# Kernel tuning notes

Hardware: AMD Instinct MI355X
Metric: run time of the kernel (lower is better)

## Reference

```python
import jax, jax.numpy as jnp
import numpy as np

VOCAB = 100000
E = 256      # embedding dim == projection dim (required by layer-axis concat)
H = 2048     # lstm hidden dim
P = 256      # projection dim
B, T = 8, 96
CELL_CLIP = 3.0
PROJ_CLIP = 3.0
NUM_LAYERS = 2


def setup_inputs() -> dict:
    key = jax.random.key(0)
    ks = jax.random.split(key, 8)
    tokens = jax.random.randint(ks[0], (B, T), 0, VOCAB, dtype=jnp.int32)
    mask = jnp.ones((B, T, 1), dtype=jnp.float32)
    embed_table = jax.random.normal(ks[1], (VOCAB + 1, E), dtype=jnp.float32) * 0.05
    # stacked LSTM weights: index 0=fwd L0, 1=fwd L1, 2=bwd L0, 3=bwd L1
    Wk = jax.random.normal(ks[2], (4, E, 4 * H), dtype=jnp.float32) * 0.02
    Wr = jax.random.normal(ks[3], (4, P, 4 * H), dtype=jnp.float32) * 0.02
    b = jnp.zeros((4, 4 * H), dtype=jnp.float32)
    Wp = jax.random.normal(ks[4], (4, H, P), dtype=jnp.float32) * 0.02
    elmo_w = jnp.zeros((NUM_LAYERS + 1,), dtype=jnp.float32)
    gamma = jnp.ones((1,), dtype=jnp.float32)
    return {"tokens": tokens, "mask": mask, "embed_table": embed_table,
            "Wk": Wk, "Wr": Wr, "b": b, "Wp": Wp,
            "elmo_w": elmo_w, "gamma": gamma}


def _lstm_proj(x, m, Wk, Wr, b, Wp, reverse):
    # x: [B,T,E], m: [B,T,1]. LSTM with cell clip, output projection, proj clip.
    if reverse:
        x = jnp.flip(x, 1)
        m = jnp.flip(m, 1)
    xs = jnp.swapaxes(x, 0, 1)                     # [T,B,E]
    ms = jnp.swapaxes(m, 0, 1)                     # [T,B,1]
    xW = jnp.einsum('tbe,ef->tbf', xs, Wk) + b     # precompute input gates [T,B,4H]

    def step(carry, inp):
        h, c = carry                               # h:[B,P], c:[B,H]
        zx, mt = inp
        z = zx + h @ Wr                            # [B,4H]
        i, f, g, o = jnp.split(z, 4, axis=-1)
        i = jax.nn.sigmoid(i)
        f = jax.nn.sigmoid(f)
        g = jnp.tanh(g)
        o = jax.nn.sigmoid(o)
        c_new = jnp.clip(f * c + i * g, -CELL_CLIP, CELL_CLIP)
        h_new = jnp.clip((o * jnp.tanh(c_new)) @ Wp, -PROJ_CLIP, PROJ_CLIP)
        keep = mt > 0
        h_new = jnp.where(keep, h_new, h)
        c_new = jnp.where(keep, c_new, c)
        return (h_new, c_new), h_new

    h0 = jnp.zeros((x.shape[0], Wp.shape[1]), x.dtype)
    c0 = jnp.zeros((x.shape[0], Wp.shape[0]), x.dtype)
    _, hs = jax.lax.scan(step, (h0, c0), (xW, ms))
    out = jnp.swapaxes(hs, 0, 1)                   # [B,T,P]
    if reverse:
        out = jnp.flip(out, 1)
    return out


def _elmo_layers(tokens, mask, embed_table, Wk, Wr, b, Wp):
    emb = embed_table[tokens]                      # [B,T,E]
    dir_outs = []
    for rev, base in ((False, 0), (True, 2)):
        inp = emb
        outs = []
        for l in range(NUM_LAYERS):
            out = _lstm_proj(inp, mask, Wk[base + l], Wr[base + l],
                             b[base + l], Wp[base + l], rev)
            inp = inp + out if l > 0 else out      # skip connection on layer > 0
            outs.append(inp)
        dir_outs.append(outs)
    fwd, bwd = dir_outs
    layers = [jnp.concatenate([emb, emb], -1)]
    layers += [jnp.concatenate([f, bb], -1) for f, bb in zip(fwd, bwd)]
    return jnp.stack(layers, axis=1)               # [B, L+1, T, 2P]


def reference(tokens, mask, embed_table, Wk, Wr, b, Wp, elmo_w, gamma):
    all_emb = _elmo_layers(tokens, mask, embed_table, Wk, Wr, b, Wp)
    m = mask[:, None, :, :]                        # [B,1,T,1]
    num = jnp.sum(mask, axis=(1, 2))[:, None]      # [B,1]
    xm = all_emb * m
    mean = jnp.sum(xm, axis=(2, 3)) / num          # [B,L+1]
    mean = mean[:, :, None, None]
    var = jnp.sum(((xm - mean) * m) ** 2, axis=(2, 3)) / num
    var = var[:, :, None, None]
    normed = (all_emb - mean) / jnp.sqrt(var + 1e-12)
    w = jax.nn.softmax(elmo_w)[None, :, None, None]
    weighted = jnp.sum(w * normed, axis=1) * gamma  # [B,T,2P]
    return weighted
```

## Files before the change

### kernel.cpp

```cpp
#include <hip/hip_runtime.h>
#include <hip/hip_bf16.h>

#define DEVFN __device__ __forceinline__

static constexpr size_t OFF_CTRS   = 0;
static constexpr size_t OFF_FLAG   = 131072;
static constexpr size_t OFF_STATS  = 131328;
static constexpr size_t OFF_EW     = 131584;
static constexpr size_t OFF_MASK32 = 131840;
static constexpr size_t OFF_EMB    = 135168;
static constexpr size_t OFF_WPT    = 921600;
static constexpr size_t OFF_BIAS   = 9310208;
static constexpr size_t OFF_XW     = 9441280;
static constexpr size_t OFF_OUT0   = 59772928;
static constexpr size_t OFF_OUT1   = 61345792;
static constexpr size_t OFF_Y      = 62918656;
static constexpr size_t OFF_H      = 75501568;

template<int BF>
DEVFN float ldin(const void* p, size_t i) {
  if (BF) {
    unsigned short u = ((const unsigned short*)p)[i];
    return __uint_as_float(((unsigned)u) << 16);
  }
  return ((const float*)p)[i];
}
DEVFN float ldraw(const void* p, size_t i, int bf) {
  if (bf) {
    unsigned short u = ((const unsigned short*)p)[i];
    return __uint_as_float(((unsigned)u) << 16);
  }
  return ((const float*)p)[i];
}

DEVFN float sigm(float x) { return 1.f / (1.f + __expf(-x)); }
DEVFN float clip3(float x) { return fminf(fmaxf(x, -3.f), 3.f); }

__global__ void detect_k(const unsigned* mask_raw, int* flagp) {
  if (threadIdx.x == 0) *flagp = (mask_raw[0] == 0x3F800000u) ? 0 : 1;
}

template<int BF>
__global__ void convert_k(const int* flagp, const void* bias, const void* mask,
                          const void* ew, const void* gm,
                          float* bias32, float* mask32, float* ew32) {
  if (*flagp != BF) return;
  size_t i = (size_t)blockIdx.x * 256 + threadIdx.x;
  if (i >= 33540) return;
  if (i < 32768)       bias32[i] = ldin<BF>(bias, i);
  else if (i < 33536)  mask32[i - 32768] = ldin<BF>(mask, i - 32768);
  else if (i < 33539)  ew32[i - 33536]   = ldin<BF>(ew, i - 33536);
  else                 ew32[3] = ldin<BF>(gm, 0);
}

template<int BF>
__global__ void transpose_wp_k(const int* flagp, const void* Wp, float* WpT) {
  if (*flagp != BF) return;
  const int kt = blockIdx.x, pt = blockIdx.y, dl = blockIdx.z;
  __shared__ float tile[64][65];
  const int tid = threadIdx.x;
  for (int it = 0; it < 4; ++it) {
    int lin = it * 1024 + tid * 4;
    int kk = lin >> 6, pp = lin & 63;
    size_t src = ((size_t)(dl * 2048 + kt * 64 + kk)) * 256 + pt * 64 + pp;
    float v0, v1, v2, v3;
    if (BF) {
      const unsigned short* sp = (const unsigned short*)Wp + src;
      v0 = __uint_as_float(((unsigned)sp[0]) << 16);
      v1 = __uint_as_float(((unsigned)sp[1]) << 16);
      v2 = __uint_as_float(((unsigned)sp[2]) << 16);
      v3 = __uint_as_float(((unsigned)sp[3]) << 16);
    } else {
      float4 v = *(const float4*)((const float*)Wp + src);
      v0 = v.x; v1 = v.y; v2 = v.z; v3 = v.w;
    }
    tile[pp + 0][kk] = v0; tile[pp + 1][kk] = v1; tile[pp + 2][kk] = v2; tile[pp + 3][kk] = v3;
  }
  __syncthreads();
  for (int it = 0; it < 4; ++it) {
    int lin = it * 1024 + tid * 4;
    int pr = lin >> 6, kc = lin & 63;
    float4 o;
    o.x = tile[pr][kc + 0]; o.y = tile[pr][kc + 1]; o.z = tile[pr][kc + 2]; o.w = tile[pr][kc + 3];
    *(float4*)(WpT + ((size_t)(dl * 256 + pt * 64 + pr)) * 2048 + kt * 64 + kc) = o;
  }
}

template<int BF>
__global__ void gather_k(const int* flagp, const int* tokens, const void* et, float* emb) {
  if (*flagp != BF) return;
  const int bt = blockIdx.x;
  const int tok = tokens[bt];
  emb[(size_t)bt * 256 + threadIdx.x] = ldin<BF>(et, (size_t)tok * 256 + threadIdx.x);
}

template<int BF>
__global__ __launch_bounds__(256) void xw_gemm_k(
    const int* __restrict__ flagp, const float* __restrict__ x_fwd, const float* __restrict__ x_bwd,
    const void* __restrict__ Wk, const float* __restrict__ bias32, float* __restrict__ xW, int layer) {
  if (*flagp != BF) return;
  const int nt = blockIdx.x, mt = blockIdx.y, dir = blockIdx.z;
  const int dl = dir * 2 + layer;
  const float* xb = dir ? x_bwd : x_fwd;
  const int tid = threadIdx.x;

  __shared__ float As[16][68];
  __shared__ float Bs[16][68];

  float acc[4][4] = {};
  const int tx = tid & 15, ty = tid >> 4;

  const int am = tid >> 2;
  const int ak = (tid & 3) * 4;
  const int m_glob = mt * 64 + am;
  const int t_ = m_glob >> 3, b_ = m_glob & 7;
  const int tau = dir ? (95 - t_) : t_;
  const float* arow = xb + ((size_t)(b_ * 96 + tau)) * 256;

  const int bk = tid >> 4, bn = (tid & 15) * 4;

  for (int kb = 0; kb < 256; kb += 16) {
    float4 av = *(const float4*)(arow + kb + ak);
    As[ak + 0][am] = av.x; As[ak + 1][am] = av.y; As[ak + 2][am] = av.z; As[ak + 3][am] = av.w;

    size_t bidx = ((size_t)dl * 256 + (kb + bk)) * 8192 + (size_t)nt * 64 + bn;
    float b0, b1, b2, b3;
    if (BF) {
      ushort4 uv = *(const ushort4*)((const unsigned short*)Wk + bidx);
      b0 = __uint_as_float(((unsigned)uv.x) << 16);
      b1 = __uint_as_float(((unsigned)uv.y) << 16);
      b2 = __uint_as_float(((unsigned)uv.z) << 16);
      b3 = __uint_as_float(((unsigned)uv.w) << 16);
    } else {
      float4 fv = *(const float4*)((const float*)Wk + bidx);
      b0 = fv.x; b1 = fv.y; b2 = fv.z; b3 = fv.w;
    }
    Bs[bk][bn + 0] = b0; Bs[bk][bn + 1] = b1; Bs[bk][bn + 2] = b2; Bs[bk][bn + 3] = b3;
    __syncthreads();

#pragma unroll
    for (int kk = 0; kk < 16; ++kk) {
      float a0 = As[kk][ty * 4 + 0], a1 = As[kk][ty * 4 + 1], a2 = As[kk][ty * 4 + 2], a3 = As[kk][ty * 4 + 3];
      float c0 = Bs[kk][tx * 4 + 0], c1 = Bs[kk][tx * 4 + 1], c2 = Bs[kk][tx * 4 + 2], c3 = Bs[kk][tx * 4 + 3];
      acc[0][0] = fmaf(a0, c0, acc[0][0]); acc[0][1] = fmaf(a0, c1, acc[0][1]);
      acc[0][2] = fmaf(a0, c2, acc[0][2]); acc[0][3] = fmaf(a0, c3, acc[0][3]);
      acc[1][0] = fmaf(a1, c0, acc[1][0]); acc[1][1] = fmaf(a1, c1, acc[1][1]);
      acc[1][2] = fmaf(a1, c2, acc[1][2]); acc[1][3] = fmaf(a1, c3, acc[1][3]);
      acc[2][0] = fmaf(a2, c0, acc[2][0]); acc[2][1] = fmaf(a2, c1, acc[2][1]);
      acc[2][2] = fmaf(a2, c2, acc[2][2]); acc[2][3] = fmaf(a2, c3, acc[2][3]);
      acc[3][0] = fmaf(a3, c0, acc[3][0]); acc[3][1] = fmaf(a3, c1, acc[3][1]);
      acc[3][2] = fmaf(a3, c2, acc[3][2]); acc[3][3] = fmaf(a3, c3, acc[3][3]);
    }
    __syncthreads();
  }

  const int n0 = nt * 64 + tx * 4;
#pragma unroll
  for (int i = 0; i < 4; ++i) {
    int m = mt * 64 + ty * 4 + i;
    int tt = m >> 3, bb = m & 7;
    float4 o;
    o.x = acc[i][0] + bias32[dl * 8192 + n0 + 0];
    o.y = acc[i][1] + bias32[dl * 8192 + n0 + 1];
    o.z = acc[i][2] + bias32[dl * 8192 + n0 + 2];
    o.w = acc[i][3] + bias32[dl * 8192 + n0 + 3];
    *(float4*)(xW + (size_t)((dir * 96 + tt) * 8 + bb) * 8192 + n0) = o;
  }
}


__global__ __launch_bounds__(256, 2) void scan_kernel(
    const float* __restrict__ xW, const void* __restrict__ WrRaw, const int* __restrict__ flagp,
    const float* __restrict__ WpT, const float* __restrict__ mask32,
    float* __restrict__ out, float* __restrict__ hbuf, float* __restrict__ ybuf,
    int* ctrs, int layer) {
  const int tid = threadIdx.x;
  const int w = blockIdx.x;
  const int dir = w >> 8;
  const int g = w & 255;
  const int dl = dir * 2 + layer;

  __shared__ __align__(16) float wr_s[256 * 32];
  __shared__ __align__(16) float h_lds[2048];
  __shared__ float4 wp4_s[512];
  __shared__ float4 zpart[288];
  __shared__ float  z_s[32 * 9];
  __shared__ __align__(16) float xw_s[256];
  __shared__ float  mask_s[768];
  __shared__ float  c_s[64];
  __shared__ float  red_s[8];

  int* base = ctrs + (layer * 2 + dir) * 65 * 64;
  int* aline = base + (g >> 2) * 64;
  int ep = 0;
  const int bf = *flagp;

  {
    const size_t wrbase = (size_t)dl * 256 * 8192;
    for (int i = tid; i < 8192; i += 256) {
      int k = i >> 5, col = i & 31;
      wr_s[i] = ldraw(WrRaw, wrbase + (size_t)k * 8192 + (size_t)(col >> 3) * 2048 + g * 8 + (col & 7), bf);
    }
    const float4* wrow = (const float4*)(WpT + ((size_t)(dl * 256 + g)) * 2048);
    for (int i = tid; i < 512; i += 256) wp4_s[i] = wrow[i];
    for (int i = tid; i < 768; i += 256) mask_s[i] = mask32[i];
  }
  if (tid < 64) c_s[tid] = 0.f;

  const int ks = tid >> 6, colq = (tid >> 3) & 7, lb = tid & 7;
  const float4* wr4 = (const float4*)wr_s;
  const float4* xw4 = (const float4*)xw_s;
  int* myline = base + (tid & 63) * 64;

  for (int t = 0; t < 96; ++t) {
    const int tau = dir ? (95 - t) : t;
    const float* h_cur = hbuf + ((size_t)(t * 2 + dir)) * 2048;
    float* h_nxt = hbuf + ((size_t)((t + 1) * 2 + dir)) * 2048;
    float* y_t   = ybuf + ((size_t)(t * 2 + dir)) * 16384;

    float xwv;
    {
      int b = tid >> 5, col = tid & 31;
      xwv = xW[(size_t)((dir * 96 + t) * 8 + b) * 8192 + (col >> 3) * 2048 + g * 8 + (col & 7)];
    }

    if (t == 0) {
      ((float4*)h_lds)[tid * 2 + 0] = make_float4(0.f, 0.f, 0.f, 0.f);
      ((float4*)h_lds)[tid * 2 + 1] = make_float4(0.f, 0.f, 0.f, 0.f);
    } else {
      ((float4*)h_lds)[tid * 2 + 0] = ((const float4*)h_cur)[tid * 2 + 0];
      ((float4*)h_lds)[tid * 2 + 1] = ((const float4*)h_cur)[tid * 2 + 1];
    }
    __syncthreads();

    {
      float4 acc = make_float4(0.f, 0.f, 0.f, 0.f);
#pragma unroll 16
      for (int i = 0; i < 64; ++i) {
        int k = (ks << 6) + i;
        float hv = h_lds[k * 8 + lb];
        float4 wv = wr4[k * 8 + colq];
        acc.x = fmaf(hv, wv.x, acc.x); acc.y = fmaf(hv, wv.y, acc.y);
        acc.z = fmaf(hv, wv.z, acc.z); acc.w = fmaf(hv, wv.w, acc.w);
      }
      zpart[(ks * 8 + colq) * 9 + lb] = acc;
      xw_s[tid] = xwv;
    }
    __syncthreads();

    ++ep;
    if (tid < 64) {
      {
        const int b3 = tid & 7, cq = tid >> 3;
        float4 z0 = zpart[(0 * 8 + cq) * 9 + b3];
        float4 z1 = zpart[(1 * 8 + cq) * 9 + b3];
        float4 z2 = zpart[(2 * 8 + cq) * 9 + b3];
        float4 z3 = zpart[(3 * 8 + cq) * 9 + b3];
        float4 xv = xw4[b3 * 8 + cq];
        z_s[(cq * 4 + 0) * 9 + b3] = z0.x + z1.x + z2.x + z3.x + xv.x;
        z_s[(cq * 4 + 1) * 9 + b3] = z0.y + z1.y + z2.y + z3.y + xv.y;
        z_s[(cq * 4 + 2) * 9 + b3] = z0.z + z1.z + z2.z + z3.z + xv.z;
        z_s[(cq * 4 + 3) * 9 + b3] = z0.w + z1.w + z2.w + z3.w + xv.w;
        const int cell = cq;
        float zi = z_s[(0  + cell) * 9 + b3];
        float zf = z_s[(8  + cell) * 9 + b3];
        float zg = z_s[(16 + cell) * 9 + b3];
        float zo = z_s[(24 + cell) * 9 + b3];
        float ig = sigm(zi), fg = sigm(zf), gg = tanhf(zg), og = sigm(zo);
        float cold = c_s[tid];
        float cc = clip3(fg * cold + ig * gg);
        float yv = og * tanhf(cc);
        float m = mask_s[b3 * 96 + tau];
        c_s[tid] = (m > 0.f) ? cc : cold;
        __hip_atomic_store(&y_t[b3 * 2048 + g * 8 + cell], yv, __ATOMIC_RELAXED, __HIP_MEMORY_SCOPE_AGENT);
      }
      asm volatile("s_waitcnt vmcnt(0)" ::: "memory");
      if (tid == 0)
        __hip_atomic_fetch_add(aline, 1, __ATOMIC_RELAXED, __HIP_MEMORY_SCOPE_AGENT);
      const int tgt = 4 * ep;
      int v = __hip_atomic_load(myline, __ATOMIC_RELAXED, __HIP_MEMORY_SCOPE_AGENT);
      while (!__all(v >= tgt)) {
        __builtin_amdgcn_s_sleep(1);
        v = __hip_atomic_load(myline, __ATOMIC_RELAXED, __HIP_MEMORY_SCOPE_AGENT);
      }
    }
    __syncthreads();

    {
      const int b = tid >> 5, kq = tid & 31;
      const float4* yb = (const float4*)y_t + b * 512;
      float s = 0.f;
#pragma unroll 8
      for (int i = 0; i < 16; ++i) {
        int k4 = i * 32 + kq;
        float4 yv = yb[k4];
        float4 wv = wp4_s[k4];
        s = fmaf(yv.x, wv.x, s); s = fmaf(yv.y, wv.y, s);
        s = fmaf(yv.z, wv.z, s); s = fmaf(yv.w, wv.w, s);
      }
      s += __shfl_down(s, 16, 32);
      s += __shfl_down(s, 8, 32);
      s += __shfl_down(s, 4, 32);
      s += __shfl_down(s, 2, 32);
      s += __shfl_down(s, 1, 32);
      if (kq == 0) red_s[b] = s;
    }
    __syncthreads();

    ++ep;
    if (tid < 64) {
      if (tid < 8) {
        float hc = clip3(red_s[tid]);
        float m = mask_s[tid * 96 + tau];
        float hp = h_lds[g * 8 + tid];
        float hv = (m > 0.f) ? hc : hp;
        __hip_atomic_store(&h_nxt[g * 8 + tid], hv, __ATOMIC_RELAXED, __HIP_MEMORY_SCOPE_AGENT);
        out[(size_t)((dir * 8 + tid) * 96 + tau) * 256 + g] = hv;
      }
      asm volatile("s_waitcnt vmcnt(0)" ::: "memory");
      if (tid == 0)
        __hip_atomic_fetch_add(aline, 1, __ATOMIC_RELAXED, __HIP_MEMORY_SCOPE_AGENT);
      const int tgt = 4 * ep;
      int v = __hip_atomic_load(myline, __ATOMIC_RELAXED, __HIP_MEMORY_SCOPE_AGENT);
      while (!__all(v >= tgt)) {
        __builtin_amdgcn_s_sleep(1);
        v = __hip_atomic_load(myline, __ATOMIC_RELAXED, __HIP_MEMORY_SCOPE_AGENT);
      }
    }
    __syncthreads();
  }
}

DEVFN float layer_val(int l, int b, int t, int f, const float* emb, const float* out0, const float* out1) {
  const int half = f >> 8, p = f & 255;
  if (l == 0) return emb[(size_t)(b * 96 + t) * 256 + p];
  const size_t o = ((size_t)((half * 8 + b) * 96 + t)) * 256 + p;
  float v = out0[o];
  if (l == 2) v += out1[o];
  return v;
}

__global__ void mixA_k(const float* emb, const float* out0, const float* out1,
                       const float* mask32, float* stats) {
  const int b = blockIdx.x / 3, l = blockIdx.x % 3;
  float s1 = 0.f, s2 = 0.f;
  for (int idx = threadIdx.x; idx < 96 * 512; idx += 256) {
    int t = idx >> 9, f = idx & 511;
    float v = layer_val(l, b, t, f, emb, out0, out1);
    float m = mask32[b * 96 + t];
    s1 += m * v; s2 += m * v * v;
  }
  for (int off = 32; off; off >>= 1) { s1 += __shfl_down(s1, off); s2 += __shfl_down(s2, off); }
  __shared__ float p1[4], p2[4];
  if ((threadIdx.x & 63) == 0) { p1[threadIdx.x >> 6] = s1; p2[threadIdx.x >> 6] = s2; }
  __syncthreads();
  if (threadIdx.x == 0) {
    float S1 = p1[0] + p1[1] + p1[2] + p1[3];
    float S2 = p2[0] + p2[1] + p2[2] + p2[3];
    float num = 0.f;
    for (int t = 0; t < 96; ++t) num += mask32[b * 96 + t];
    float mean = S1 / num;
    float var = S2 / num - 2.f * mean * mean + 512.f * mean * mean;
    stats[(b * 3 + l) * 2 + 0] = mean;
    stats[(b * 3 + l) * 2 + 1] = rsqrtf(var + 1e-12f);
  }
}

__global__ void mixB_k(const int* flagp, const float* emb, const float* out0, const float* out1,
                       const float* stats, const float* ew32, void* outp) {
  const int idx = blockIdx.x * 256 + threadIdx.x;
  const int b = idx / 49152;
  const int r = idx % 49152;
  const int t = r >> 9, f = r & 511;
  float w0 = ew32[0], w1 = ew32[1], w2 = ew32[2], gm = ew32[3];
  float mx = fmaxf(w0, fmaxf(w1, w2));
  float e0 = __expf(w0 - mx), e1 = __expf(w1 - mx), e2 = __expf(w2 - mx);
  float inv = 1.f / (e0 + e1 + e2);
  float wl[3] = {e0 * inv, e1 * inv, e2 * inv};
  float acc = 0.f;
#pragma unroll
  for (int l = 0; l < 3; ++l) {
    float v = layer_val(l, b, t, f, emb, out0, out1);
    acc += wl[l] * (v - stats[(b * 3 + l) * 2]) * stats[(b * 3 + l) * 2 + 1];
  }
  acc *= gm;
  if (*flagp) ((__hip_bfloat16*)outp)[idx] = __float2bfloat16(acc);
  else        ((float*)outp)[idx] = acc;
}

extern "C" void kernel_launch(void* const* d_in, const int* in_sizes, int n_in,
                              void* d_out, int out_size, void* d_ws, size_t ws_size,
                              hipStream_t stream) {
  const int*  tokens = (const int*)d_in[0];
  const void* maskp  = d_in[1];
  const void* embt   = d_in[2];
  const void* Wk     = d_in[3];
  const void* WrRaw  = d_in[4];
  const void* bias   = d_in[5];
  const void* Wp     = d_in[6];
  const void* ew     = d_in[7];
  const void* gm     = d_in[8];

  char* ws = (char*)d_ws;
  int*   ctrs   = (int*)(ws + OFF_CTRS);
  int*   flagp  = (int*)(ws + OFF_FLAG);
  float* stats  = (float*)(ws + OFF_STATS);
  float* ew32   = (float*)(ws + OFF_EW);
  float* mask32 = (float*)(ws + OFF_MASK32);
  float* emb    = (float*)(ws + OFF_EMB);
  float* wpt    = (float*)(ws + OFF_WPT);
  float* bias32 = (float*)(ws + OFF_BIAS);
  float* xW     = (float*)(ws + OFF_XW);
  float* out0   = (float*)(ws + OFF_OUT0);
  float* out1   = (float*)(ws + OFF_OUT1);
  float* ybuf   = (float*)(ws + OFF_Y);
  float* hbuf   = (float*)(ws + OFF_H);

  hipMemsetAsync(d_ws, 0, 131072, stream);
  detect_k<<<1, 64, 0, stream>>>((const unsigned*)maskp, flagp);

  convert_k<0><<<132, 256, 0, stream>>>(flagp, bias, maskp, ew, gm, bias32, mask32, ew32);
  convert_k<1><<<132, 256, 0, stream>>>(flagp, bias, maskp, ew, gm, bias32, mask32, ew32);

  transpose_wp_k<0><<<dim3(32, 4, 4), 256, 0, stream>>>(flagp, Wp, wpt);
  transpose_wp_k<1><<<dim3(32, 4, 4), 256, 0, stream>>>(flagp, Wp, wpt);

  gather_k<0><<<768, 256, 0, stream>>>(flagp, tokens, embt, emb);
  gather_k<1><<<768, 256, 0, stream>>>(flagp, tokens, embt, emb);

  xw_gemm_k<0><<<dim3(128, 12, 2), 256, 0, stream>>>(flagp, emb, emb, Wk, bias32, xW, 0);
  xw_gemm_k<1><<<dim3(128, 12, 2), 256, 0, stream>>>(flagp, emb, emb, Wk, bias32, xW, 0);

  int l0 = 0, l1 = 1;
  {
    void* args[] = {&xW, &WrRaw, &flagp, &wpt, &mask32, &out0, &hbuf, &ybuf, &ctrs, &l0};
    hipError_t e = hipLaunchCooperativeKernel((void*)scan_kernel, dim3(512), dim3(256), args, 0, stream);
    if (e != hipSuccess)
      scan_kernel<<<512, 256, 0, stream>>>(xW, WrRaw, flagp, wpt, mask32, out0, hbuf, ybuf, ctrs, 0);
  }

  float* x_fwd = out0;
  float* x_bwd = out0 + (size_t)8 * 96 * 256;
  xw_gemm_k<0><<<dim3(128, 12, 2), 256, 0, stream>>>(flagp, x_fwd, x_bwd, Wk, bias32, xW, 1);
  xw_gemm_k<1><<<dim3(128, 12, 2), 256, 0, stream>>>(flagp, x_fwd, x_bwd, Wk, bias32, xW, 1);

  {
    void* args[] = {&xW, &WrRaw, &flagp, &wpt, &mask32, &out1, &hbuf, &ybuf, &ctrs, &l1};
    hipError_t e = hipLaunchCooperativeKernel((void*)scan_kernel, dim3(512), dim3(256), args, 0, stream);
    if (e != hipSuccess)
      scan_kernel<<<512, 256, 0, stream>>>(xW, WrRaw, flagp, wpt, mask32, out1, hbuf, ybuf, ctrs, 1);
  }

  mixA_k<<<24, 256, 0, stream>>>(emb, out0, out1, mask32, stats);
  mixB_k<<<1536, 256, 0, stream>>>(flagp, emb, out0, out1, stats, ew32, d_out);
}
```

Baseline: 2.416 ms.

## Replace counter-based grid barrier with flat per-block epoch slots and fuse prep kernels

The per-step inter-block barrier in the recurrent scan changes from atomic fetch-add counters to per-block epoch stores. Each wave now polls four slots per lane, which removes atomic contention on shared counter lines and shortens the critical path of each of the many barriers per layer. The output write after the h update moves past the barrier so it no longer delays signalling. Separately, the dtype-detect, convert, Wp-transpose and gather kernels are merged into one prep kernel, and the dtype is detected inline from the mask, cutting launch overhead. In exchange, every waiting wave now issues more polling loads.

```diff
diff --git a/kernel.cpp b/kernel.cpp
--- a/kernel.cpp
+++ b/kernel.cpp
@@ -4,7 +4,6 @@
 #define DEVFN __device__ __forceinline__
 
 static constexpr size_t OFF_CTRS   = 0;
-static constexpr size_t OFF_FLAG   = 131072;
 static constexpr size_t OFF_STATS  = 131328;
 static constexpr size_t OFF_EW     = 131584;
 static constexpr size_t OFF_MASK32 = 131840;
@@ -36,69 +35,71 @@
 DEVFN float sigm(float x) { return 1.f / (1.f + __expf(-x)); }
 DEVFN float clip3(float x) { return fminf(fmaxf(x, -3.f), 3.f); }
 
-__global__ void detect_k(const unsigned* mask_raw, int* flagp) {
-  if (threadIdx.x == 0) *flagp = (mask_raw[0] == 0x3F800000u) ? 0 : 1;
+DEVFN int detect_bf(const void* maskp) {
+  return (((const unsigned*)maskp)[0] == 0x3F800000u) ? 0 : 1;
 }
 
 template<int BF>
-__global__ void convert_k(const int* flagp, const void* bias, const void* mask,
-                          const void* ew, const void* gm,
-                          float* bias32, float* mask32, float* ew32) {
-  if (*flagp != BF) return;
-  size_t i = (size_t)blockIdx.x * 256 + threadIdx.x;
-  if (i >= 33540) return;
-  if (i < 32768)       bias32[i] = ldin<BF>(bias, i);
-  else if (i < 33536)  mask32[i - 32768] = ldin<BF>(mask, i - 32768);
-  else if (i < 33539)  ew32[i - 33536]   = ldin<BF>(ew, i - 33536);
-  else                 ew32[3] = ldin<BF>(gm, 0);
-}
-
-template<int BF>
-__global__ void transpose_wp_k(const int* flagp, const void* Wp, float* WpT) {
-  if (*flagp != BF) return;
-  const int kt = blockIdx.x, pt = blockIdx.y, dl = blockIdx.z;
-  __shared__ float tile[64][65];
-  const int tid = threadIdx.x;
-  for (int it = 0; it < 4; ++it) {
-    int lin = it * 1024 + tid * 4;
-    int kk = lin >> 6, pp = lin & 63;
-    size_t src = ((size_t)(dl * 2048 + kt * 64 + kk)) * 256 + pt * 64 + pp;
-    float v0, v1, v2, v3;
-    if (BF) {
-      const unsigned short* sp = (const unsigned short*)Wp + src;
-      v0 = __uint_as_float(((unsigned)sp[0]) << 16);
-      v1 = __uint_as_float(((unsigned)sp[1]) << 16);
-      v2 = __uint_as_float(((unsigned)sp[2]) << 16);
-      v3 = __uint_as_float(((unsigned)sp[3]) << 16);
-    } else {
-      float4 v = *(const float4*)((const float*)Wp + src);
-      v0 = v.x; v1 = v.y; v2 = v.z; v3 = v.w;
-    }
-    tile[pp + 0][kk] = v0; tile[pp + 1][kk] = v1; tile[pp + 2][kk] = v2; tile[pp + 3][kk] = v3;
-  }
-  __syncthreads();
-  for (int it = 0; it < 4; ++it) {
-    int lin = it * 1024 + tid * 4;
-    int pr = lin >> 6, kc = lin & 63;
-    float4 o;
-    o.x = tile[pr][kc + 0]; o.y = tile[pr][kc + 1]; o.z = tile[pr][kc + 2]; o.w = tile[pr][kc + 3];
-    *(float4*)(WpT + ((size_t)(dl * 256 + pt * 64 + pr)) * 2048 + kt * 64 + kc) = o;
-  }
-}
-
-template<int BF>
-__global__ void gather_k(const int* flagp, const int* tokens, const void* et, float* emb) {
-  if (*flagp != BF) return;
-  const int bt = blockIdx.x;
+__global__ void prep_k(const int* __restrict__ tokens, const void* __restrict__ maskp,
+                       const void* __restrict__ et, const void* __restrict__ bias,
+                       const void* __restrict__ ew, const void* __restrict__ gm,
+                       const void* __restrict__ Wp,
+                       float* bias32, float* mask32, float* ew32, float* emb, float* WpT) {
+  if (detect_bf(maskp) != BF) return;
+  const int bid = blockIdx.x, tid = threadIdx.x;
+
+  if (bid < 132) {
+    size_t i = (size_t)bid * 256 + tid;
+    if (i >= 33540) return;
+    if (i < 32768)       bias32[i] = ldin<BF>(bias, i);
+    else if (i < 33536)  mask32[i - 32768] = ldin<BF>(maskp, i - 32768);
+    else if (i < 33539)  ew32[i - 33536]   = ldin<BF>(ew, i - 33536);
+    else                 ew32[3] = ldin<BF>(gm, 0);
+    return;
+  }
+
+  if (bid < 644) {
+    const int r = bid - 132;
+    const int kt = r & 31, pt = (r >> 5) & 3, dl = r >> 7;
+    __shared__ float tile[64][65];
+    for (int it = 0; it < 4; ++it) {
+      int lin = it * 1024 + tid * 4;
+      int kk = lin >> 6, pp = lin & 63;
+      size_t src = ((size_t)(dl * 2048 + kt * 64 + kk)) * 256 + pt * 64 + pp;
+      float v0, v1, v2, v3;
+      if (BF) {
+        const unsigned short* sp = (const unsigned short*)Wp + src;
+        v0 = __uint_as_float(((unsigned)sp[0]) << 16);
+        v1 = __uint_as_float(((unsigned)sp[1]) << 16);
+        v2 = __uint_as_float(((unsigned)sp[2]) << 16);
+        v3 = __uint_as_float(((unsigned)sp[3]) << 16);
+      } else {
+        float4 v = *(const float4*)((const float*)Wp + src);
+        v0 = v.x; v1 = v.y; v2 = v.z; v3 = v.w;
+      }
+      tile[pp + 0][kk] = v0; tile[pp + 1][kk] = v1; tile[pp + 2][kk] = v2; tile[pp + 3][kk] = v3;
+    }
+    __syncthreads();
+    for (int it = 0; it < 4; ++it) {
+      int lin = it * 1024 + tid * 4;
+      int pr = lin >> 6, kc = lin & 63;
+      float4 o;
+      o.x = tile[pr][kc + 0]; o.y = tile[pr][kc + 1]; o.z = tile[pr][kc + 2]; o.w = tile[pr][kc + 3];
+      *(float4*)(WpT + ((size_t)(dl * 256 + pt * 64 + pr)) * 2048 + kt * 64 + kc) = o;
+    }
+    return;
+  }
+
+  const int bt = bid - 644;
   const int tok = tokens[bt];
-  emb[(size_t)bt * 256 + threadIdx.x] = ldin<BF>(et, (size_t)tok * 256 + threadIdx.x);
+  emb[(size_t)bt * 256 + tid] = ldin<BF>(et, (size_t)tok * 256 + tid);
 }
 
 template<int BF>
 __global__ __launch_bounds__(256) void xw_gemm_k(
-    const int* __restrict__ flagp, const float* __restrict__ x_fwd, const float* __restrict__ x_bwd,
+    const void* __restrict__ maskp, const float* __restrict__ x_fwd, const float* __restrict__ x_bwd,
     const void* __restrict__ Wk, const float* __restrict__ bias32, float* __restrict__ xW, int layer) {
-  if (*flagp != BF) return;
+  if (detect_bf(maskp) != BF) return;
   const int nt = blockIdx.x, mt = blockIdx.y, dir = blockIdx.z;
   const int dl = dir * 2 + layer;
   const float* xb = dir ? x_bwd : x_fwd;
@@ -168,9 +169,21 @@
   }
 }
 
+DEVFN void flat_poll(const int* slots, int tid, int ep) {
+  const int* a = slots + tid * 16;
+  for (;;) {
+    int v0 = __hip_atomic_load(a + 0,  __ATOMIC_RELAXED, __HIP_MEMORY_SCOPE_AGENT);
+    int v1 = __hip_atomic_load(a + 4,  __ATOMIC_RELAXED, __HIP_MEMORY_SCOPE_AGENT);
+    int v2 = __hip_atomic_load(a + 8,  __ATOMIC_RELAXED, __HIP_MEMORY_SCOPE_AGENT);
+    int v3 = __hip_atomic_load(a + 12, __ATOMIC_RELAXED, __HIP_MEMORY_SCOPE_AGENT);
+    bool ok = (v0 >= ep) & (v1 >= ep) & (v2 >= ep) & (v3 >= ep);
+    if (__all(ok)) break;
+    __builtin_amdgcn_s_sleep(1);
+  }
+}
 
 __global__ __launch_bounds__(256, 2) void scan_kernel(
-    const float* __restrict__ xW, const void* __restrict__ WrRaw, const int* __restrict__ flagp,
+    const float* __restrict__ xW, const void* __restrict__ WrRaw, const void* __restrict__ maskp,
     const float* __restrict__ WpT, const float* __restrict__ mask32,
     float* __restrict__ out, float* __restrict__ hbuf, float* __restrict__ ybuf,
     int* ctrs, int layer) {
@@ -190,10 +203,10 @@
   __shared__ float  c_s[64];
   __shared__ float  red_s[8];
 
-  int* base = ctrs + (layer * 2 + dir) * 65 * 64;
-  int* aline = base + (g >> 2) * 64;
+  int* slots  = ctrs + (layer * 2 + dir) * 4096;
+  int* myslot = slots + g * 4;
   int ep = 0;
-  const int bf = *flagp;
+  const int bf = detect_bf(maskp);
 
   {
     const size_t wrbase = (size_t)dl * 256 * 8192;
@@ -210,7 +223,6 @@
   const int ks = tid >> 6, colq = (tid >> 3) & 7, lb = tid & 7;
   const float4* wr4 = (const float4*)wr_s;
   const float4* xw4 = (const float4*)xw_s;
-  int* myline = base + (tid & 63) * 64;
 
   for (int t = 0; t < 96; ++t) {
     const int tau = dir ? (95 - t) : t;
@@ -276,13 +288,8 @@
       }
       asm volatile("s_waitcnt vmcnt(0)" ::: "memory");
       if (tid == 0)
-        __hip_atomic_fetch_add(aline, 1, __ATOMIC_RELAXED, __HIP_MEMORY_SCOPE_AGENT);
-      const int tgt = 4 * ep;
-      int v = __hip_atomic_load(myline, __ATOMIC_RELAXED, __HIP_MEMORY_SCOPE_AGENT);
-      while (!__all(v >= tgt)) {
-        __builtin_amdgcn_s_sleep(1);
-        v = __hip_atomic_load(myline, __ATOMIC_RELAXED, __HIP_MEMORY_SCOPE_AGENT);
-      }
+        __hip_atomic_store(myslot, ep, __ATOMIC_RELAXED, __HIP_MEMORY_SCOPE_AGENT);
+      flat_poll(slots, tid, ep);
     }
     __syncthreads();
 
@@ -309,23 +316,20 @@
 
     ++ep;
     if (tid < 64) {
+      float hv = 0.f;
       if (tid < 8) {
         float hc = clip3(red_s[tid]);
         float m = mask_s[tid * 96 + tau];
         float hp = h_lds[g * 8 + tid];
-        float hv = (m > 0.f) ? hc : hp;
+        hv = (m > 0.f) ? hc : hp;
         __hip_atomic_store(&h_nxt[g * 8 + tid], hv, __ATOMIC_RELAXED, __HIP_MEMORY_SCOPE_AGENT);
-        out[(size_t)((dir * 8 + tid) * 96 + tau) * 256 + g] = hv;
       }
       asm volatile("s_waitcnt vmcnt(0)" ::: "memory");
       if (tid == 0)
-        __hip_atomic_fetch_add(aline, 1, __ATOMIC_RELAXED, __HIP_MEMORY_SCOPE_AGENT);
-      const int tgt = 4 * ep;
-      int v = __hip_atomic_load(myline, __ATOMIC_RELAXED, __HIP_MEMORY_SCOPE_AGENT);
-      while (!__all(v >= tgt)) {
-        __builtin_amdgcn_s_sleep(1);
-        v = __hip_atomic_load(myline, __ATOMIC_RELAXED, __HIP_MEMORY_SCOPE_AGENT);
-      }
+        __hip_atomic_store(myslot, ep, __ATOMIC_RELAXED, __HIP_MEMORY_SCOPE_AGENT);
+      flat_poll(slots, tid, ep);
+      if (tid < 8)
+        out[(size_t)((dir * 8 + tid) * 96 + tau) * 256 + g] = hv;
     }
     __syncthreads();
   }
@@ -366,7 +370,7 @@
   }
 }
 
-__global__ void mixB_k(const int* flagp, const float* emb, const float* out0, const float* out1,
+__global__ void mixB_k(const void* maskp, const float* emb, const float* out0, const float* out1,
                        const float* stats, const float* ew32, void* outp) {
   const int idx = blockIdx.x * 256 + threadIdx.x;
   const int b = idx / 49152;
@@ -384,8 +388,8 @@
     acc += wl[l] * (v - stats[(b * 3 + l) * 2]) * stats[(b * 3 + l) * 2 + 1];
   }
   acc *= gm;
-  if (*flagp) ((__hip_bfloat16*)outp)[idx] = __float2bfloat16(acc);
-  else        ((float*)outp)[idx] = acc;
+  if (detect_bf(maskp)) ((__hip_bfloat16*)outp)[idx] = __float2bfloat16(acc);
+  else                  ((float*)outp)[idx] = acc;
 }
 
 extern "C" void kernel_launch(void* const* d_in, const int* in_sizes, int n_in,
@@ -403,7 +407,6 @@
 
   char* ws = (char*)d_ws;
   int*   ctrs   = (int*)(ws + OFF_CTRS);
-  int*   flagp  = (int*)(ws + OFF_FLAG);
   float* stats  = (float*)(ws + OFF_STATS);
   float* ew32   = (float*)(ws + OFF_EW);
   float* mask32 = (float*)(ws + OFF_MASK32);
@@ -417,40 +420,35 @@
   float* hbuf   = (float*)(ws + OFF_H);
 
   hipMemsetAsync(d_ws, 0, 131072, stream);
-  detect_k<<<1, 64, 0, stream>>>((const unsigned*)maskp, flagp);
-
-  convert_k<0><<<132, 256, 0, stream>>>(flagp, bias, maskp, ew, gm, bias32, mask32, ew32);
-  convert_k<1><<<132, 256, 0, stream>>>(flagp, bias, maskp, ew, gm, bias32, mask32, ew32);
-
-  transpose_wp_k<0><<<dim3(32, 4, 4), 256, 0, stream>>>(flagp, Wp, wpt);
-  transpose_wp_k<1><<<dim3(32, 4, 4), 256, 0, stream>>>(flagp, Wp, wpt);
-
-  gather_k<0><<<768, 256, 0, stream>>>(flagp, tokens, embt, emb);
-  gather_k<1><<<768, 256, 0, stream>>>(flagp, tokens, embt, emb);
-
-  xw_gemm_k<0><<<dim3(128, 12, 2), 256, 0, stream>>>(flagp, emb, emb, Wk, bias32, xW, 0);
-  xw_gemm_k<1><<<dim3(128, 12, 2), 256, 0, stream>>>(flagp, emb, emb, Wk, bias32, xW, 0);
+
+  prep_k<0><<<1412, 256, 0, stream>>>(tokens, maskp, embt, bias, ew, gm, Wp,
+                                      bias32, mask32, ew32, emb, wpt);
+  prep_k<1><<<1412, 256, 0, stream>>>(tokens, maskp, embt, bias, ew, gm, Wp,
+                                      bias32, mask32, ew32, emb, wpt);
+
+  xw_gemm_k<0><<<dim3(128, 12, 2), 256, 0, stream>>>(maskp, emb, emb, Wk, bias32, xW, 0);
+  xw_gemm_k<1><<<dim3(128, 12, 2), 256, 0, stream>>>(maskp, emb, emb, Wk, bias32, xW, 0);
 
   int l0 = 0, l1 = 1;
   {
-    void* args[] = {&xW, &WrRaw, &flagp, &wpt, &mask32, &out0, &hbuf, &ybuf, &ctrs, &l0};
+    void* args[] = {&xW, &WrRaw, &maskp, &wpt, &mask32, &out0, &hbuf, &ybuf, &ctrs, &l0};
     hipError_t e = hipLaunchCooperativeKernel((void*)scan_kernel, dim3(512), dim3(256), args, 0, stream);
     if (e != hipSuccess)
-      scan_kernel<<<512, 256, 0, stream>>>(xW, WrRaw, flagp, wpt, mask32, out0, hbuf, ybuf, ctrs, 0);
+      scan_kernel<<<512, 256, 0, stream>>>(xW, WrRaw, maskp, wpt, mask32, out0, hbuf, ybuf, ctrs, 0);
   }
 
   float* x_fwd = out0;
   float* x_bwd = out0 + (size_t)8 * 96 * 256;
-  xw_gemm_k<0><<<dim3(128, 12, 2), 256, 0, stream>>>(flagp, x_fwd, x_bwd, Wk, bias32, xW, 1);
-  xw_gemm_k<1><<<dim3(128, 12, 2), 256, 0, stream>>>(flagp, x_fwd, x_bwd, Wk, bias32, xW, 1);
+  xw_gemm_k<0><<<dim3(128, 12, 2), 256, 0, stream>>>(maskp, x_fwd, x_bwd, Wk, bias32, xW, 1);
+  xw_gemm_k<1><<<dim3(128, 12, 2), 256, 0, stream>>>(maskp, x_fwd, x_bwd, Wk, bias32, xW, 1);
 
   {
-    void* args[] = {&xW, &WrRaw, &flagp, &wpt, &mask32, &out1, &hbuf, &ybuf, &ctrs, &l1};
+    void* args[] = {&xW, &WrRaw, &maskp, &wpt, &mask32, &out1, &hbuf, &ybuf, &ctrs, &l1};
     hipError_t e = hipLaunchCooperativeKernel((void*)scan_kernel, dim3(512), dim3(256), args, 0, stream);
     if (e != hipSuccess)
-      scan_kernel<<<512, 256, 0, stream>>>(xW, WrRaw, flagp, wpt, mask32, out1, hbuf, ybuf, ctrs, 1);
+      scan_kernel<<<512, 256, 0, stream>>>(xW, WrRaw, maskp, wpt, mask32, out1, hbuf, ybuf, ctrs, 1);
   }
 
   mixA_k<<<24, 256, 0, stream>>>(emb, out0, out1, mask32, stats);
-  mixB_k<<<1536, 256, 0, stream>>>(flagp, emb, out0, out1, stats, ew32, d_out);
-}
+  mixB_k<<<1536, 256, 0, stream>>>(maskp, emb, out0, out1, stats, ew32, d_out);
+}
```

New measurement: 2.742 ms. 1.13x slower.
